# Kernel tuning notes

Hardware: AMD Instinct MI355X
Metric: run time of the kernel (lower is better)

Reference implementation:

```python
import jax, jax.numpy as jnp
import numpy as np

TOP_K = 8


def setup_inputs() -> dict:
    key = jax.random.key(0)
    ks = jax.random.split(key, 5)
    T, H, I, E = 4096, 2048, 1024, 64
    s = 0.02
    return {
        "x": jax.random.normal(ks[0], (T, H), jnp.float32),
        "gate_w": jax.random.normal(ks[1], (E, H), jnp.float32) * s,
        "gate_b": jax.random.normal(ks[2], (E,), jnp.float32) * s,
        "fc1_w": jax.random.normal(ks[3], (E, 2 * I, H), jnp.float32) * s,
        "fc2_w": jax.random.normal(ks[4], (E, H, I), jnp.float32) * s,
    }


def reference(x, gate_w, gate_b, fc1_w, fc2_w):
    # Router: [T, E] logits, top-k, softmax over selected logits in fp32.
    E = gate_w.shape[0]
    logits = x @ gate_w.T + gate_b
    topk_logits, topk_idx = jax.lax.top_k(logits, TOP_K)
    w = jax.nn.softmax(topk_logits.astype(jnp.float32), axis=-1).astype(x.dtype)
    # Per-token combine weight for each expert: [T, E] (0 if expert not selected).
    comb = (jax.nn.one_hot(topk_idx, E, dtype=x.dtype) * w[..., None]).sum(axis=1)
    # Scan over experts: each step is one dense GEMM-GeGLU-GEMM with masked combine.
    def body(acc, ew):
        W1, W2, c = ew  # W1 [2I, H], W2 [H, I], c [T]
        h_full = x @ W1.T                       # [T, 2I]
        h, g = jnp.split(h_full, 2, axis=-1)
        a = jax.nn.gelu(h, approximate=False) * (g + 1.0)  # custom GeGLU
        y = a @ W2.T                            # [T, H]
        return acc + c[:, None] * y, None

    out0 = jnp.zeros_like(x)
    out, _ = jax.lax.scan(body, out0, (fc1_w, fc2_w, comb.T))
    return out
```

## Files before the change

kernel.cpp:

```cpp
#include <hip/hip_runtime.h>
#include <hip/hip_bf16.h>
#include <cfloat>
#include <math.h>

#define T_TOK 4096
#define H_DIM 2048
#define E_NUM 64
#define I_DIM 1024
#define TOPK  8
#define BM    256
#define BK    64
#define MAXT  192

typedef __attribute__((ext_vector_type(4))) float f32x4;
typedef __attribute__((ext_vector_type(8))) short bf16x8;
typedef __attribute__((ext_vector_type(4))) int   i32x4;

__device__ __forceinline__ unsigned short f2bf(float f) {
    union { float f; unsigned int u; } v; v.f = f;
    unsigned int r = v.u + 0x7FFFu + ((v.u >> 16) & 1u);
    return (unsigned short)(r >> 16);
}
__device__ __forceinline__ unsigned int pack2(float a, float b) {
    return (unsigned int)f2bf(a) | ((unsigned int)f2bf(b) << 16);
}
__device__ __forceinline__ float bf2f(unsigned short u) {
    union { unsigned int u; float f; } v; v.u = (unsigned int)u << 16; return v.f;
}
__device__ __forceinline__ int cvtpk(float lo, float hi) {
    int r; asm("v_cvt_pk_bf16_f32 %0, %1, %2" : "=v"(r) : "v"(lo), "v"(hi)); return r;
}
__device__ __forceinline__ void gload16(const void* g, void* l) {
    __builtin_amdgcn_global_load_lds((const __attribute__((address_space(1))) unsigned int*)g,
                                     (__attribute__((address_space(3))) unsigned int*)l, 16, 0, 0);
}

__global__ __launch_bounds__(256)
void router_kernel(const float* __restrict__ x, const float* __restrict__ gw,
                   const float* __restrict__ gb, unsigned short* __restrict__ xb,
                   int* __restrict__ topk_idx, float* __restrict__ topk_w,
                   int* __restrict__ counts)
{
    const int t = blockIdx.x;
    const int tid = threadIdx.x;
    __shared__ float xs[H_DIM];
    __shared__ float logits[E_NUM];
    const float* xrow = x + (size_t)t * H_DIM;

    #pragma unroll
    for (int i = 0; i < 2; ++i) {
        int c = i * 1024 + tid * 4;
        f32x4 v = *(const f32x4*)(xrow + c);
        *(f32x4*)(xs + c) = v;
        uint2 pk; pk.x = pack2(v.x, v.y); pk.y = pack2(v.z, v.w);
        *(uint2*)(xb + (size_t)t * H_DIM + c) = pk;
    }
    __syncthreads();

    const int wave = tid >> 6, lane = tid & 63;
    for (int ee = 0; ee < 16; ++ee) {
        const int e = wave * 16 + ee;
        const float* g = gw + (size_t)e * H_DIM;
        float p = 0.f;
        #pragma unroll
        for (int i = 0; i < 8; ++i) {
            int c = (i * 64 + lane) * 4;
            f32x4 gv = *(const f32x4*)(g + c);
            f32x4 xv = *(const f32x4*)(xs + c);
            p += gv.x * xv.x + gv.y * xv.y + gv.z * xv.z + gv.w * xv.w;
        }
        #pragma unroll
        for (int s = 32; s > 0; s >>= 1) p += __shfl_xor(p, s, 64);
        if (lane == 0) logits[e] = p + gb[e];
    }
    __syncthreads();

    if (tid < 64) {
        float cur = logits[tid];
        float wv[TOPK]; int wi[TOPK];
        #pragma unroll
        for (int k = 0; k < TOPK; ++k) {
            float bv = cur; int bi = tid;
            #pragma unroll
            for (int s = 32; s > 0; s >>= 1) {
                float ov = __shfl_xor(bv, s, 64);
                int   oi = __shfl_xor(bi, s, 64);
                if (ov > bv || (ov == bv && oi < bi)) { bv = ov; bi = oi; }
            }
            wv[k] = bv; wi[k] = bi;
            if (tid == bi) cur = -FLT_MAX;
        }
        if (tid == 0) {
            float mx = wv[0], sum = 0.f, ex[TOPK];
            #pragma unroll
            for (int k = 0; k < TOPK; ++k) { ex[k] = expf(wv[k] - mx); sum += ex[k]; }
            #pragma unroll
            for (int k = 0; k < TOPK; ++k) {
                topk_idx[t * TOPK + k] = wi[k];
                topk_w[t * TOPK + k]   = ex[k] / sum;
                atomicAdd(&counts[wi[k]], 1);
            }
        }
    }
}

__global__ void scan_kernel(const int* __restrict__ counts, int* __restrict__ offsets,
                            int* __restrict__ cursors, int* __restrict__ tiles,
                            int* __restrict__ ntiles)
{
    if (threadIdx.x == 0) {
        int acc = 0, nt = 0;
        for (int e = 0; e < E_NUM; ++e) {
            offsets[e] = acc; cursors[e] = acc;
            int c = counts[e];
            for (int m = 0; m * BM < c; ++m) tiles[nt++] = (e << 16) | m;
            acc += c;
        }
        *ntiles = nt;
    }
}

__global__ void assign_kernel(const int* __restrict__ topk_idx, const float* __restrict__ topk_w,
                              int* __restrict__ cursors, int* __restrict__ tok_of,
                              int* __restrict__ pos_of)
{
    int i = blockIdx.x * 256 + threadIdx.x;
    if (i >= T_TOK * TOPK) return;
    int e = topk_idx[i];
    int pos = atomicAdd(&cursors[e], 1);
    tok_of[pos] = i >> 3;
    pos_of[i]   = pos;
}

__global__ __launch_bounds__(512, 1)
void gemm1_kernel(const unsigned short* __restrict__ xb, const float* __restrict__ fc1,
                  const int* __restrict__ counts, const int* __restrict__ offsets,
                  const int* __restrict__ tok_of, const int* __restrict__ tiles,
                  const int* __restrict__ ntiles, unsigned short* __restrict__ a_all)
{
    const int ty = blockIdx.y;
    if (ty >= *ntiles) return;
    const int code = tiles[ty];
    const int e = code >> 16, m0 = (code & 0xffff) * BM;
    const int cnt = counts[e], off = offsets[e];
    const int n0 = blockIdx.x * 128;
    const float* W = fc1 + (size_t)e * (size_t)(2 * I_DIM) * H_DIM;

    __shared__ unsigned short sA[2][BM * BK];
    __shared__ unsigned short sB[2 * 128 * BK];
    __shared__ int sTok[BM];

    const int tid = threadIdx.x;
    if (tid < BM) {
        int m = m0 + tid;
        sTok[tid] = tok_of[off + (m < cnt ? m : cnt - 1)];
    }
    __syncthreads();

    const int wid = tid >> 6, lane = tid & 63;
    const int srow = tid >> 3, sch = tid & 7;
    const int sslot = sch ^ (srow & 7);

    const unsigned short* aSrc[4];
    const float* bSrc[4];
    #pragma unroll
    for (int i = 0; i < 4; ++i) {
        int row = srow + 64 * i;
        aSrc[i] = xb + (size_t)sTok[row] * H_DIM + sslot * 8;
        int wrow = (row < 128) ? (n0 + row) : (I_DIM + n0 + (row - 128));
        bSrc[i] = W + (size_t)wrow * H_DIM + sch * 8;
    }

    f32x4 accH[4][4], accG[4][4];
    #pragma unroll
    for (int m = 0; m < 4; ++m)
        #pragma unroll
        for (int n = 0; n < 4; ++n) {
            accH[m][n] = (f32x4){0.f, 0.f, 0.f, 0.f};
            accG[m][n] = (f32x4){0.f, 0.f, 0.f, 0.f};
        }

    const int wm = (wid >> 1) * 64;
    const int wnp = (wid & 1) * 64;
    const int fr = lane & 15;
    const int kg = lane >> 4;

    f32x4 br[8];

    auto issueB = [&](int k0) {
        #pragma unroll
        for (int i = 0; i < 4; ++i) {
            br[2 * i]     = *(const f32x4*)(bSrc[i] + k0);
            br[2 * i + 1] = *(const f32x4*)(bSrc[i] + k0 + 4);
        }
    };
    auto issueA = [&](int k0, int buf) {
        #pragma unroll
        for (int i = 0; i < 4; ++i)
            gload16(aSrc[i] + k0, &sA[buf][(64 * i + 8 * wid) * BK]);
    };
    auto writeB = [&]() {
        #pragma unroll
        for (int i = 0; i < 4; ++i) {
            int row = srow + 64 * i;
            i32x4 pk = (i32x4){cvtpk(br[2*i].x,   br[2*i].y),
                               cvtpk(br[2*i].z,   br[2*i].w),
                               cvtpk(br[2*i+1].x, br[2*i+1].y),
                               cvtpk(br[2*i+1].z, br[2*i+1].w)};
            int byte = (row * 128 + sch * 16) ^ ((row & 7) << 4);
            *(i32x4*)((char*)sB + byte) = pk;
        }
    };
    auto compute = [&](int buf) {
        #pragma unroll
        for (int kk = 0; kk < 2; ++kk) {
            bf16x8 af[4], bh[4], bg[4];
            #pragma unroll
            for (int m = 0; m < 4; ++m) {
                int row = wm + m * 16 + fr;
                af[m] = *(const bf16x8*)((const char*)sA[buf] +
                        ((row * 128 + kk * 64 + kg * 16) ^ ((row & 7) << 4)));
            }
            #pragma unroll
            for (int n = 0; n < 4; ++n) {
                int rh = wnp + n * 16 + fr;
                bh[n] = *(const bf16x8*)((const char*)sB +
                        ((rh * 128 + kk * 64 + kg * 16) ^ ((rh & 7) << 4)));
                int rg = 128 + rh;
                bg[n] = *(const bf16x8*)((const char*)sB +
                        ((rg * 128 + kk * 64 + kg * 16) ^ ((rg & 7) << 4)));
            }
            #pragma unroll
            for (int m = 0; m < 4; ++m)
                #pragma unroll
                for (int n = 0; n < 4; ++n) {
                    accH[m][n] = __builtin_amdgcn_mfma_f32_16x16x32_bf16(af[m], bh[n], accH[m][n], 0, 0, 0);
                    accG[m][n] = __builtin_amdgcn_mfma_f32_16x16x32_bf16(af[m], bg[n], accG[m][n], 0, 0, 0);
                }
        }
    };

    const int NT = H_DIM / BK;
    issueB(0);
    issueA(0, 0);
    __syncthreads();
    writeB();
    __syncthreads();
    int cur = 0;
    for (int t = 0; t < NT; ++t) {
        const bool more = (t + 1) < NT;
        if (more) { issueB((t + 1) * BK); issueA((t + 1) * BK, cur ^ 1); }
        compute(cur);
        __syncthreads();
        if (more) writeB();
        __syncthreads();
        cur ^= 1;
    }

    #pragma unroll
    for (int m = 0; m < 4; ++m) {
        int rbase = wm + m * 16 + kg * 4;
        #pragma unroll
        for (int r = 0; r < 4; ++r) {
            int gm = m0 + rbase + r;
            if (gm < cnt) {
                size_t rowoff = (size_t)(off + gm) * I_DIM + n0 + wnp;
                #pragma unroll
                for (int n = 0; n < 4; ++n) {
                    float h = accH[m][n][r];
                    float g = accG[m][n][r];
                    float a = 0.5f * h * (1.f + erff(h * 0.70710678118f)) * (g + 1.f);
                    a_all[rowoff + n * 16 + fr] = f2bf(a);
                }
            }
        }
    }
}

__global__ __launch_bounds__(512, 1)
void gemm2_kernel(const unsigned short* __restrict__ a_all, const float* __restrict__ fc2,
                  const int* __restrict__ counts, const int* __restrict__ offsets,
                  const int* __restrict__ tiles, const int* __restrict__ ntiles,
                  unsigned short* __restrict__ y)
{
    const int ty = blockIdx.y;
    if (ty >= *ntiles) return;
    const int code = tiles[ty];
    const int e = code >> 16, m0 = (code & 0xffff) * BM;
    const int cnt = counts[e], off = offsets[e];
    const int n0 = blockIdx.x * 128;
    const float* W = fc2 + (size_t)e * (size_t)H_DIM * I_DIM;

    __shared__ unsigned short sA[2][BM * BK];
    __shared__ unsigned short sB[128 * BK];

    const int tid = threadIdx.x;
    const int wid = tid >> 6, lane = tid & 63;
    const int srow = tid >> 3, sch = tid & 7;
    const int sslot = sch ^ (srow & 7);

    const unsigned short* aSrc[4];
    const float* bSrc[2];
    #pragma unroll
    for (int i = 0; i < 4; ++i) {
        int row = srow + 64 * i;
        aSrc[i] = a_all + (size_t)(off + m0 + row) * I_DIM + sslot * 8;
    }
    #pragma unroll
    for (int i = 0; i < 2; ++i) {
        int row = srow + 64 * i;
        bSrc[i] = W + (size_t)(n0 + row) * I_DIM + sch * 8;
    }

    f32x4 acc[4][4];
    #pragma unroll
    for (int m = 0; m < 4; ++m)
        #pragma unroll
        for (int n = 0; n < 4; ++n) acc[m][n] = (f32x4){0.f, 0.f, 0.f, 0.f};

    const int wm = (wid >> 1) * 64;
    const int wn = (wid & 1) * 64;
    const int fr = lane & 15;
    const int kg = lane >> 4;

    f32x4 br[4];

    auto issueB = [&](int k0) {
        #pragma unroll
        for (int i = 0; i < 2; ++i) {
            br[2 * i]     = *(const f32x4*)(bSrc[i] + k0);
            br[2 * i + 1] = *(const f32x4*)(bSrc[i] + k0 + 4);
        }
    };
    auto issueA = [&](int k0, int buf) {
        #pragma unroll
        for (int i = 0; i < 4; ++i)
            gload16(aSrc[i] + k0, &sA[buf][(64 * i + 8 * wid) * BK]);
    };
    auto writeB = [&]() {
        #pragma unroll
        for (int i = 0; i < 2; ++i) {
            int row = srow + 64 * i;
            i32x4 pk = (i32x4){cvtpk(br[2*i].x,   br[2*i].y),
                               cvtpk(br[2*i].z,   br[2*i].w),
                               cvtpk(br[2*i+1].x, br[2*i+1].y),
                               cvtpk(br[2*i+1].z, br[2*i+1].w)};
            int byte = (row * 128 + sch * 16) ^ ((row & 7) << 4);
            *(i32x4*)((char*)sB + byte) = pk;
        }
    };
    auto compute = [&](int buf) {
        #pragma unroll
        for (int kk = 0; kk < 2; ++kk) {
            bf16x8 af[4], bfr[4];
            #pragma unroll
            for (int m = 0; m < 4; ++m) {
                int row = wm + m * 16 + fr;
                af[m] = *(const bf16x8*)((const char*)sA[buf] +
                        ((row * 128 + kk * 64 + kg * 16) ^ ((row & 7) << 4)));
            }
            #pragma unroll
            for (int n = 0; n < 4; ++n) {
                int row = wn + n * 16 + fr;
                bfr[n] = *(const bf16x8*)((const char*)sB +
                        ((row * 128 + kk * 64 + kg * 16) ^ ((row & 7) << 4)));
            }
            #pragma unroll
            for (int m = 0; m < 4; ++m)
                #pragma unroll
                for (int n = 0; n < 4; ++n)
                    acc[m][n] = __builtin_amdgcn_mfma_f32_16x16x32_bf16(af[m], bfr[n], acc[m][n], 0, 0, 0);
        }
    };

    const int NT = I_DIM / BK;
    issueB(0);
    issueA(0, 0);
    __syncthreads();
    writeB();
    __syncthreads();
    int cur = 0;
    for (int t = 0; t < NT; ++t) {
        const bool more = (t + 1) < NT;
        if (more) { issueB((t + 1) * BK); issueA((t + 1) * BK, cur ^ 1); }
        compute(cur);
        __syncthreads();
        if (more) writeB();
        __syncthreads();
        cur ^= 1;
    }

    #pragma unroll
    for (int m = 0; m < 4; ++m) {
        int rbase = wm + m * 16 + kg * 4;
        #pragma unroll
        for (int r = 0; r < 4; ++r) {
            int gm = m0 + rbase + r;
            if (gm < cnt) {
                size_t rowoff = (size_t)(off + gm) * H_DIM + n0 + wn;
                #pragma unroll
                for (int n = 0; n < 4; ++n)
                    y[rowoff + n * 16 + fr] = f2bf(acc[m][n][r]);
            }
        }
    }
}

__global__ __launch_bounds__(256)
void combine_kernel(const unsigned short* __restrict__ y, const int* __restrict__ pos_of,
                    const float* __restrict__ topk_w, float* __restrict__ out)
{
    const int t = blockIdx.x;
    const int tid = threadIdx.x;
    __shared__ int   sp[TOPK];
    __shared__ float sw[TOPK];
    if (tid < TOPK) {
        sp[tid] = pos_of[t * TOPK + tid];
        sw[tid] = topk_w[t * TOPK + tid];
    }
    __syncthreads();

    const int c0 = tid * 8;
    float acc[8];
    #pragma unroll
    for (int j = 0; j < 8; ++j) acc[j] = 0.f;
    #pragma unroll
    for (int k = 0; k < TOPK; ++k) {
        const float w = sw[k];
        i32x4 v = *(const i32x4*)(y + (size_t)sp[k] * H_DIM + c0);
        const unsigned short* u = (const unsigned short*)&v;
        #pragma unroll
        for (int j = 0; j < 8; ++j) acc[j] += w * bf2f(u[j]);
    }
    float* orow = out + (size_t)t * H_DIM + c0;
    *(f32x4*)orow       = (f32x4){acc[0], acc[1], acc[2], acc[3]};
    *(f32x4*)(orow + 4) = (f32x4){acc[4], acc[5], acc[6], acc[7]};
}

extern "C" void kernel_launch(void* const* d_in, const int* in_sizes, int n_in,
                              void* d_out, int out_size, void* d_ws, size_t ws_size,
                              hipStream_t stream)
{
    const float* x   = (const float*)d_in[0];
    const float* gw  = (const float*)d_in[1];
    const float* gb  = (const float*)d_in[2];
    const float* fc1 = (const float*)d_in[3];
    const float* fc2 = (const float*)d_in[4];
    float* out = (float*)d_out;

    char* ws = (char*)d_ws;
    size_t o = 0;
    auto alloc = [&](size_t b) { void* p = ws + o; o = (o + b + 255) & ~(size_t)255; return p; };
    unsigned short* xb     = (unsigned short*)alloc((size_t)T_TOK * H_DIM * 2);
    int*            tk_idx = (int*)  alloc((size_t)T_TOK * TOPK * 4);
    float*          tk_w   = (float*)alloc((size_t)T_TOK * TOPK * 4);
    int*            counts = (int*)  alloc(E_NUM * 4);
    int*            offs   = (int*)  alloc(E_NUM * 4);
    int*            curs   = (int*)  alloc(E_NUM * 4);
    int*            tiles  = (int*)  alloc(MAXT * 4);
    int*            ntiles = (int*)  alloc(4);
    int*            tok_of = (int*)  alloc((size_t)T_TOK * TOPK * 4);
    int*            pos_of = (int*)  alloc((size_t)T_TOK * TOPK * 4);
    unsigned short* a_all  = (unsigned short*)alloc((size_t)(T_TOK * TOPK + BM) * I_DIM * 2);
    unsigned short* yb     = (unsigned short*)alloc((size_t)T_TOK * TOPK * H_DIM * 2);
    (void)ws_size;

    hipMemsetAsync(counts, 0, E_NUM * 4, stream);

    router_kernel<<<T_TOK, 256, 0, stream>>>(x, gw, gb, xb, tk_idx, tk_w, counts);
    scan_kernel<<<1, 64, 0, stream>>>(counts, offs, curs, tiles, ntiles);
    assign_kernel<<<(T_TOK * TOPK + 255) / 256, 256, 0, stream>>>(tk_idx, tk_w, curs, tok_of, pos_of);
    gemm1_kernel<<<dim3(I_DIM / 128, MAXT), 512, 0, stream>>>(xb, fc1, counts, offs, tok_of,
                                                              tiles, ntiles, a_all);
    gemm2_kernel<<<dim3(H_DIM / 128, MAXT), 512, 0, stream>>>(a_all, fc2, counts, offs,
                                                              tiles, ntiles, yb);
    combine_kernel<<<T_TOK, 256, 0, stream>>>(yb, pos_of, tk_w, out);
}
```

Baseline: 1.261 ms.

## Use 640-row expert tiles so most experts fit one M tile, single-buffer A

Raises the per-expert M tile from 256 to 640 rows, so a typical expert (about 512 tokens) needs one tile and the fp32 weights are streamed and converted once per expert rather than per 256-row tile. Each warp now owns 80 rows. gemm1's N tile shrinks to 64 and gemm2's per-warp N grows to 128. To fit LDS, A moves from double to single buffering, with the A load issued after compute, which serialises A loads with MFMA work. Risks include wasted padding rows and worse latency hiding.

Measured after the change: 1.145 ms. 1.1x faster.

```diff
diff --git a/kernel.cpp b/kernel.cpp
--- a/kernel.cpp
+++ b/kernel.cpp
@@ -8,9 +8,9 @@
 #define E_NUM 64
 #define I_DIM 1024
 #define TOPK  8
-#define BM    256
+#define BM    640
 #define BK    64
-#define MAXT  192
+#define MAXT  128
 
 typedef __attribute__((ext_vector_type(4))) float f32x4;
 typedef __attribute__((ext_vector_type(8))) short bf16x8;
@@ -143,17 +143,21 @@
     const int code = tiles[ty];
     const int e = code >> 16, m0 = (code & 0xffff) * BM;
     const int cnt = counts[e], off = offsets[e];
-    const int n0 = blockIdx.x * 128;
+    const int n0 = blockIdx.x * 64;
     const float* W = fc1 + (size_t)e * (size_t)(2 * I_DIM) * H_DIM;
 
-    __shared__ unsigned short sA[2][BM * BK];
-    __shared__ unsigned short sB[2 * 128 * BK];
+    __shared__ unsigned short sA[BM * BK];
+    __shared__ unsigned short sB[128 * BK];
     __shared__ int sTok[BM];
 
     const int tid = threadIdx.x;
-    if (tid < BM) {
-        int m = m0 + tid;
-        sTok[tid] = tok_of[off + (m < cnt ? m : cnt - 1)];
+    {
+        int r0 = m0 + tid;
+        sTok[tid] = tok_of[off + (r0 < cnt ? r0 : cnt - 1)];
+        if (tid < BM - 512) {
+            int r1 = m0 + 512 + tid;
+            sTok[512 + tid] = tok_of[off + (r1 < cnt ? r1 : cnt - 1)];
+        }
     }
     __syncthreads();
 
@@ -161,165 +165,30 @@
     const int srow = tid >> 3, sch = tid & 7;
     const int sslot = sch ^ (srow & 7);
 
-    const unsigned short* aSrc[4];
-    const float* bSrc[4];
-    #pragma unroll
-    for (int i = 0; i < 4; ++i) {
+    const unsigned short* aSrc[10];
+    #pragma unroll
+    for (int i = 0; i < 10; ++i) {
         int row = srow + 64 * i;
         aSrc[i] = xb + (size_t)sTok[row] * H_DIM + sslot * 8;
-        int wrow = (row < 128) ? (n0 + row) : (I_DIM + n0 + (row - 128));
+    }
+    const float* bSrc[2];
+    #pragma unroll
+    for (int i = 0; i < 2; ++i) {
+        int row = srow + 64 * i;
+        int wrow = (row < 64) ? (n0 + row) : (I_DIM + n0 + (row - 64));
         bSrc[i] = W + (size_t)wrow * H_DIM + sch * 8;
     }
 
-    f32x4 accH[4][4], accG[4][4];
-    #pragma unroll
-    for (int m = 0; m < 4; ++m)
+    f32x4 accH[5][4], accG[5][4];
+    #pragma unroll
+    for (int m = 0; m < 5; ++m)
         #pragma unroll
         for (int n = 0; n < 4; ++n) {
             accH[m][n] = (f32x4){0.f, 0.f, 0.f, 0.f};
             accG[m][n] = (f32x4){0.f, 0.f, 0.f, 0.f};
         }
 
-    const int wm = (wid >> 1) * 64;
-    const int wnp = (wid & 1) * 64;
-    const int fr = lane & 15;
-    const int kg = lane >> 4;
-
-    f32x4 br[8];
-
-    auto issueB = [&](int k0) {
-        #pragma unroll
-        for (int i = 0; i < 4; ++i) {
-            br[2 * i]     = *(const f32x4*)(bSrc[i] + k0);
-            br[2 * i + 1] = *(const f32x4*)(bSrc[i] + k0 + 4);
-        }
-    };
-    auto issueA = [&](int k0, int buf) {
-        #pragma unroll
-        for (int i = 0; i < 4; ++i)
-            gload16(aSrc[i] + k0, &sA[buf][(64 * i + 8 * wid) * BK]);
-    };
-    auto writeB = [&]() {
-        #pragma unroll
-        for (int i = 0; i < 4; ++i) {
-            int row = srow + 64 * i;
-            i32x4 pk = (i32x4){cvtpk(br[2*i].x,   br[2*i].y),
-                               cvtpk(br[2*i].z,   br[2*i].w),
-                               cvtpk(br[2*i+1].x, br[2*i+1].y),
-                               cvtpk(br[2*i+1].z, br[2*i+1].w)};
-            int byte = (row * 128 + sch * 16) ^ ((row & 7) << 4);
-            *(i32x4*)((char*)sB + byte) = pk;
-        }
-    };
-    auto compute = [&](int buf) {
-        #pragma unroll
-        for (int kk = 0; kk < 2; ++kk) {
-            bf16x8 af[4], bh[4], bg[4];
-            #pragma unroll
-            for (int m = 0; m < 4; ++m) {
-                int row = wm + m * 16 + fr;
-                af[m] = *(const bf16x8*)((const char*)sA[buf] +
-                        ((row * 128 + kk * 64 + kg * 16) ^ ((row & 7) << 4)));
-            }
-            #pragma unroll
-            for (int n = 0; n < 4; ++n) {
-                int rh = wnp + n * 16 + fr;
-                bh[n] = *(const bf16x8*)((const char*)sB +
-                        ((rh * 128 + kk * 64 + kg * 16) ^ ((rh & 7) << 4)));
-                int rg = 128 + rh;
-                bg[n] = *(const bf16x8*)((const char*)sB +
-                        ((rg * 128 + kk * 64 + kg * 16) ^ ((rg & 7) << 4)));
-            }
-            #pragma unroll
-            for (int m = 0; m < 4; ++m)
-                #pragma unroll
-                for (int n = 0; n < 4; ++n) {
-                    accH[m][n] = __builtin_amdgcn_mfma_f32_16x16x32_bf16(af[m], bh[n], accH[m][n], 0, 0, 0);
-                    accG[m][n] = __builtin_amdgcn_mfma_f32_16x16x32_bf16(af[m], bg[n], accG[m][n], 0, 0, 0);
-                }
-        }
-    };
-
-    const int NT = H_DIM / BK;
-    issueB(0);
-    issueA(0, 0);
-    __syncthreads();
-    writeB();
-    __syncthreads();
-    int cur = 0;
-    for (int t = 0; t < NT; ++t) {
-        const bool more = (t + 1) < NT;
-        if (more) { issueB((t + 1) * BK); issueA((t + 1) * BK, cur ^ 1); }
-        compute(cur);
-        __syncthreads();
-        if (more) writeB();
-        __syncthreads();
-        cur ^= 1;
-    }
-
-    #pragma unroll
-    for (int m = 0; m < 4; ++m) {
-        int rbase = wm + m * 16 + kg * 4;
-        #pragma unroll
-        for (int r = 0; r < 4; ++r) {
-            int gm = m0 + rbase + r;
-            if (gm < cnt) {
-                size_t rowoff = (size_t)(off + gm) * I_DIM + n0 + wnp;
-                #pragma unroll
-                for (int n = 0; n < 4; ++n) {
-                    float h = accH[m][n][r];
-                    float g = accG[m][n][r];
-                    float a = 0.5f * h * (1.f + erff(h * 0.70710678118f)) * (g + 1.f);
-                    a_all[rowoff + n * 16 + fr] = f2bf(a);
-                }
-            }
-        }
-    }
-}
-
-__global__ __launch_bounds__(512, 1)
-void gemm2_kernel(const unsigned short* __restrict__ a_all, const float* __restrict__ fc2,
-                  const int* __restrict__ counts, const int* __restrict__ offsets,
-                  const int* __restrict__ tiles, const int* __restrict__ ntiles,
-                  unsigned short* __restrict__ y)
-{
-    const int ty = blockIdx.y;
-    if (ty >= *ntiles) return;
-    const int code = tiles[ty];
-    const int e = code >> 16, m0 = (code & 0xffff) * BM;
-    const int cnt = counts[e], off = offsets[e];
-    const int n0 = blockIdx.x * 128;
-    const float* W = fc2 + (size_t)e * (size_t)H_DIM * I_DIM;
-
-    __shared__ unsigned short sA[2][BM * BK];
-    __shared__ unsigned short sB[128 * BK];
-
-    const int tid = threadIdx.x;
-    const int wid = tid >> 6, lane = tid & 63;
-    const int srow = tid >> 3, sch = tid & 7;
-    const int sslot = sch ^ (srow & 7);
-
-    const unsigned short* aSrc[4];
-    const float* bSrc[2];
-    #pragma unroll
-    for (int i = 0; i < 4; ++i) {
-        int row = srow + 64 * i;
-        aSrc[i] = a_all + (size_t)(off + m0 + row) * I_DIM + sslot * 8;
-    }
-    #pragma unroll
-    for (int i = 0; i < 2; ++i) {
-        int row = srow + 64 * i;
-        bSrc[i] = W + (size_t)(n0 + row) * I_DIM + sch * 8;
-    }
-
-    f32x4 acc[4][4];
-    #pragma unroll
-    for (int m = 0; m < 4; ++m)
-        #pragma unroll
-        for (int n = 0; n < 4; ++n) acc[m][n] = (f32x4){0.f, 0.f, 0.f, 0.f};
-
-    const int wm = (wid >> 1) * 64;
-    const int wn = (wid & 1) * 64;
+    const int wm = wid * 80;
     const int fr = lane & 15;
     const int kg = lane >> 4;
 
@@ -332,10 +201,10 @@
             br[2 * i + 1] = *(const f32x4*)(bSrc[i] + k0 + 4);
         }
     };
-    auto issueA = [&](int k0, int buf) {
-        #pragma unroll
-        for (int i = 0; i < 4; ++i)
-            gload16(aSrc[i] + k0, &sA[buf][(64 * i + 8 * wid) * BK]);
+    auto issueA = [&](int k0) {
+        #pragma unroll
+        for (int i = 0; i < 10; ++i)
+            gload16(aSrc[i] + k0, &sA[(64 * i + 8 * wid) * BK]);
     };
     auto writeB = [&]() {
         #pragma unroll
@@ -349,57 +218,188 @@
             *(i32x4*)((char*)sB + byte) = pk;
         }
     };
-    auto compute = [&](int buf) {
+    auto compute = [&]() {
         #pragma unroll
         for (int kk = 0; kk < 2; ++kk) {
-            bf16x8 af[4], bfr[4];
-            #pragma unroll
-            for (int m = 0; m < 4; ++m) {
+            bf16x8 af[5], bh[4], bg[4];
+            #pragma unroll
+            for (int m = 0; m < 5; ++m) {
                 int row = wm + m * 16 + fr;
-                af[m] = *(const bf16x8*)((const char*)sA[buf] +
+                af[m] = *(const bf16x8*)((const char*)sA +
                         ((row * 128 + kk * 64 + kg * 16) ^ ((row & 7) << 4)));
             }
             #pragma unroll
             for (int n = 0; n < 4; ++n) {
-                int row = wn + n * 16 + fr;
-                bfr[n] = *(const bf16x8*)((const char*)sB +
-                        ((row * 128 + kk * 64 + kg * 16) ^ ((row & 7) << 4)));
-            }
-            #pragma unroll
-            for (int m = 0; m < 4; ++m)
+                int rh = n * 16 + fr;
+                bh[n] = *(const bf16x8*)((const char*)sB +
+                        ((rh * 128 + kk * 64 + kg * 16) ^ ((rh & 7) << 4)));
+                int rg = 64 + rh;
+                bg[n] = *(const bf16x8*)((const char*)sB +
+                        ((rg * 128 + kk * 64 + kg * 16) ^ ((rg & 7) << 4)));
+            }
+            #pragma unroll
+            for (int m = 0; m < 5; ++m)
                 #pragma unroll
-                for (int n = 0; n < 4; ++n)
-                    acc[m][n] = __builtin_amdgcn_mfma_f32_16x16x32_bf16(af[m], bfr[n], acc[m][n], 0, 0, 0);
-        }
-    };
-
-    const int NT = I_DIM / BK;
+                for (int n = 0; n < 4; ++n) {
+                    accH[m][n] = __builtin_amdgcn_mfma_f32_16x16x32_bf16(af[m], bh[n], accH[m][n], 0, 0, 0);
+                    accG[m][n] = __builtin_amdgcn_mfma_f32_16x16x32_bf16(af[m], bg[n], accG[m][n], 0, 0, 0);
+                }
+        }
+    };
+
+    const int NT = H_DIM / BK;
     issueB(0);
-    issueA(0, 0);
+    issueA(0);
     __syncthreads();
     writeB();
     __syncthreads();
-    int cur = 0;
     for (int t = 0; t < NT; ++t) {
-        const bool more = (t + 1) < NT;
-        if (more) { issueB((t + 1) * BK); issueA((t + 1) * BK, cur ^ 1); }
-        compute(cur);
+        if (t + 1 < NT) issueB((t + 1) * BK);
+        compute();
         __syncthreads();
-        if (more) writeB();
+        if (t + 1 < NT) { issueA((t + 1) * BK); writeB(); }
         __syncthreads();
-        cur ^= 1;
-    }
-
-    #pragma unroll
-    for (int m = 0; m < 4; ++m) {
+    }
+
+    #pragma unroll
+    for (int m = 0; m < 5; ++m) {
         int rbase = wm + m * 16 + kg * 4;
         #pragma unroll
         for (int r = 0; r < 4; ++r) {
             int gm = m0 + rbase + r;
             if (gm < cnt) {
-                size_t rowoff = (size_t)(off + gm) * H_DIM + n0 + wn;
+                size_t rowoff = (size_t)(off + gm) * I_DIM + n0;
                 #pragma unroll
-                for (int n = 0; n < 4; ++n)
+                for (int n = 0; n < 4; ++n) {
+                    float h = accH[m][n][r];
+                    float g = accG[m][n][r];
+                    float a = 0.5f * h * (1.f + erff(h * 0.70710678118f)) * (g + 1.f);
+                    a_all[rowoff + n * 16 + fr] = f2bf(a);
+                }
+            }
+        }
+    }
+}
+
+__global__ __launch_bounds__(512, 1)
+void gemm2_kernel(const unsigned short* __restrict__ a_all, const float* __restrict__ fc2,
+                  const int* __restrict__ counts, const int* __restrict__ offsets,
+                  const int* __restrict__ tiles, const int* __restrict__ ntiles,
+                  unsigned short* __restrict__ y)
+{
+    const int ty = blockIdx.y;
+    if (ty >= *ntiles) return;
+    const int code = tiles[ty];
+    const int e = code >> 16, m0 = (code & 0xffff) * BM;
+    const int cnt = counts[e], off = offsets[e];
+    const int n0 = blockIdx.x * 128;
+    const float* W = fc2 + (size_t)e * (size_t)H_DIM * I_DIM;
+
+    __shared__ unsigned short sA[BM * BK];
+    __shared__ unsigned short sB[128 * BK];
+
+    const int tid = threadIdx.x;
+    const int wid = tid >> 6, lane = tid & 63;
+    const int srow = tid >> 3, sch = tid & 7;
+    const int sslot = sch ^ (srow & 7);
+
+    const unsigned short* aSrc[10];
+    #pragma unroll
+    for (int i = 0; i < 10; ++i) {
+        int row = srow + 64 * i;
+        aSrc[i] = a_all + (size_t)(off + m0 + row) * I_DIM + sslot * 8;
+    }
+    const float* bSrc[2];
+    #pragma unroll
+    for (int i = 0; i < 2; ++i) {
+        int row = srow + 64 * i;
+        bSrc[i] = W + (size_t)(n0 + row) * I_DIM + sch * 8;
+    }
+
+    f32x4 acc[5][8];
+    #pragma unroll
+    for (int m = 0; m < 5; ++m)
+        #pragma unroll
+        for (int n = 0; n < 8; ++n) acc[m][n] = (f32x4){0.f, 0.f, 0.f, 0.f};
+
+    const int wm = wid * 80;
+    const int fr = lane & 15;
+    const int kg = lane >> 4;
+
+    f32x4 br[4];
+
+    auto issueB = [&](int k0) {
+        #pragma unroll
+        for (int i = 0; i < 2; ++i) {
+            br[2 * i]     = *(const f32x4*)(bSrc[i] + k0);
+            br[2 * i + 1] = *(const f32x4*)(bSrc[i] + k0 + 4);
+        }
+    };
+    auto issueA = [&](int k0) {
+        #pragma unroll
+        for (int i = 0; i < 10; ++i)
+            gload16(aSrc[i] + k0, &sA[(64 * i + 8 * wid) * BK]);
+    };
+    auto writeB = [&]() {
+        #pragma unroll
+        for (int i = 0; i < 2; ++i) {
+            int row = srow + 64 * i;
+            i32x4 pk = (i32x4){cvtpk(br[2*i].x,   br[2*i].y),
+                               cvtpk(br[2*i].z,   br[2*i].w),
+                               cvtpk(br[2*i+1].x, br[2*i+1].y),
+                               cvtpk(br[2*i+1].z, br[2*i+1].w)};
+            int byte = (row * 128 + sch * 16) ^ ((row & 7) << 4);
+            *(i32x4*)((char*)sB + byte) = pk;
+        }
+    };
+    auto compute = [&]() {
+        #pragma unroll
+        for (int kk = 0; kk < 2; ++kk) {
+            bf16x8 af[5], bfr[8];
+            #pragma unroll
+            for (int m = 0; m < 5; ++m) {
+                int row = wm + m * 16 + fr;
+                af[m] = *(const bf16x8*)((const char*)sA +
+                        ((row * 128 + kk * 64 + kg * 16) ^ ((row & 7) << 4)));
+            }
+            #pragma unroll
+            for (int n = 0; n < 8; ++n) {
+                int row = n * 16 + fr;
+                bfr[n] = *(const bf16x8*)((const char*)sB +
+                        ((row * 128 + kk * 64 + kg * 16) ^ ((row & 7) << 4)));
+            }
+            #pragma unroll
+            for (int m = 0; m < 5; ++m)
+                #pragma unroll
+                for (int n = 0; n < 8; ++n)
+                    acc[m][n] = __builtin_amdgcn_mfma_f32_16x16x32_bf16(af[m], bfr[n], acc[m][n], 0, 0, 0);
+        }
+    };
+
+    const int NT = I_DIM / BK;
+    issueB(0);
+    issueA(0);
+    __syncthreads();
+    writeB();
+    __syncthreads();
+    for (int t = 0; t < NT; ++t) {
+        if (t + 1 < NT) issueB((t + 1) * BK);
+        compute();
+        __syncthreads();
+        if (t + 1 < NT) { issueA((t + 1) * BK); writeB(); }
+        __syncthreads();
+    }
+
+    #pragma unroll
+    for (int m = 0; m < 5; ++m) {
+        int rbase = wm + m * 16 + kg * 4;
+        #pragma unroll
+        for (int r = 0; r < 4; ++r) {
+            int gm = m0 + rbase + r;
+            if (gm < cnt) {
+                size_t rowoff = (size_t)(off + gm) * H_DIM + n0;
+                #pragma unroll
+                for (int n = 0; n < 8; ++n)
                     y[rowoff + n * 16 + fr] = f2bf(acc[m][n][r]);
             }
         }
@@ -462,7 +462,7 @@
     int*            tok_of = (int*)  alloc((size_t)T_TOK * TOPK * 4);
     int*            pos_of = (int*)  alloc((size_t)T_TOK * TOPK * 4);
     unsigned short* a_all  = (unsigned short*)alloc((size_t)(T_TOK * TOPK + BM) * I_DIM * 2);
-    unsigned short* yb     = (unsigned short*)alloc((size_t)T_TOK * TOPK * H_DIM * 2);
+    unsigned short* yb     = (unsigned short*)alloc((size_t)(T_TOK * TOPK + BM) * H_DIM * 2);
     (void)ws_size;
 
     hipMemsetAsync(counts, 0, E_NUM * 4, stream);
@@ -470,8 +470,8 @@
     router_kernel<<<T_TOK, 256, 0, stream>>>(x, gw, gb, xb, tk_idx, tk_w, counts);
     scan_kernel<<<1, 64, 0, stream>>>(counts, offs, curs, tiles, ntiles);
     assign_kernel<<<(T_TOK * TOPK + 255) / 256, 256, 0, stream>>>(tk_idx, tk_w, curs, tok_of, pos_of);
-    gemm1_kernel<<<dim3(I_DIM / 128, MAXT), 512, 0, stream>>>(xb, fc1, counts, offs, tok_of,
-                                                              tiles, ntiles, a_all);
+    gemm1_kernel<<<dim3(I_DIM / 64, MAXT), 512, 0, stream>>>(xb, fc1, counts, offs, tok_of,
+                                                             tiles, ntiles, a_all);
     gemm2_kernel<<<dim3(H_DIM / 128, MAXT), 512, 0, stream>>>(a_all, fc2, counts, offs,
                                                               tiles, ntiles, yb);
     combine_kernel<<<T_TOK, 256, 0, stream>>>(yb, pos_of, tk_w, out);
```

## Shrink grouped GEMM tiles to 128x128, split GeGLU into separate kernel

Applied to the files above, without the earlier changes.

Both expert GEMMs move from 256-row tiles with 512 threads to 128x128 tiles with 256 threads and two blocks per CU. The B tile is now double-buffered so one barrier per k-step can be dropped, and MFMA sections are wrapped in s_setprio. GEMM1 no longer pairs the h and g halves in one block. It writes the full bf16 pre-activation to a new buffer, and a separate elementwise kernel applies the GeGLU. The goal is less padding waste per expert and better occupancy, at the cost of extra global traffic for the intermediate and one more launch.

Result: slower. 1.501 ms (+19.0%).

```diff
diff --git a/kernel.cpp b/kernel.cpp
--- a/kernel.cpp
+++ b/kernel.cpp
@@ -8,9 +8,9 @@
 #define E_NUM 64
 #define I_DIM 1024
 #define TOPK  8
-#define BM    256
+#define BM    128
 #define BK    64
-#define MAXT  192
+#define MAXT  320
 
 typedef __attribute__((ext_vector_type(4))) float f32x4;
 typedef __attribute__((ext_vector_type(8))) short bf16x8;
@@ -132,22 +132,22 @@
     pos_of[i]   = pos;
 }
 
-__global__ __launch_bounds__(512, 1)
+__global__ __launch_bounds__(256, 2)
 void gemm1_kernel(const unsigned short* __restrict__ xb, const float* __restrict__ fc1,
                   const int* __restrict__ counts, const int* __restrict__ offsets,
                   const int* __restrict__ tok_of, const int* __restrict__ tiles,
-                  const int* __restrict__ ntiles, unsigned short* __restrict__ a_all)
+                  const int* __restrict__ ntiles, unsigned short* __restrict__ h_full)
 {
     const int ty = blockIdx.y;
     if (ty >= *ntiles) return;
     const int code = tiles[ty];
     const int e = code >> 16, m0 = (code & 0xffff) * BM;
     const int cnt = counts[e], off = offsets[e];
-    const int n0 = blockIdx.x * 128;
+    const int n0 = blockIdx.x * BM;
     const float* W = fc1 + (size_t)e * (size_t)(2 * I_DIM) * H_DIM;
 
     __shared__ unsigned short sA[2][BM * BK];
-    __shared__ unsigned short sB[2 * 128 * BK];
+    __shared__ unsigned short sB[2][BM * BK];
     __shared__ int sTok[BM];
 
     const int tid = threadIdx.x;
@@ -159,29 +159,24 @@
 
     const int wid = tid >> 6, lane = tid & 63;
     const int srow = tid >> 3, sch = tid & 7;
-    const int sslot = sch ^ (srow & 7);
+    const int brow = tid >> 1, bhalf = tid & 1;
 
     const unsigned short* aSrc[4];
-    const float* bSrc[4];
     #pragma unroll
     for (int i = 0; i < 4; ++i) {
-        int row = srow + 64 * i;
-        aSrc[i] = xb + (size_t)sTok[row] * H_DIM + sslot * 8;
-        int wrow = (row < 128) ? (n0 + row) : (I_DIM + n0 + (row - 128));
-        bSrc[i] = W + (size_t)wrow * H_DIM + sch * 8;
-    }
-
-    f32x4 accH[4][4], accG[4][4];
+        int row = srow + 32 * i;
+        aSrc[i] = xb + (size_t)sTok[row] * H_DIM + (sch ^ (row & 7)) * 8;
+    }
+    const float* bSrc = W + (size_t)(n0 + brow) * H_DIM + bhalf * 32;
+
+    f32x4 acc[4][4];
     #pragma unroll
     for (int m = 0; m < 4; ++m)
         #pragma unroll
-        for (int n = 0; n < 4; ++n) {
-            accH[m][n] = (f32x4){0.f, 0.f, 0.f, 0.f};
-            accG[m][n] = (f32x4){0.f, 0.f, 0.f, 0.f};
-        }
+        for (int n = 0; n < 4; ++n) acc[m][n] = (f32x4){0.f, 0.f, 0.f, 0.f};
 
     const int wm = (wid >> 1) * 64;
-    const int wnp = (wid & 1) * 64;
+    const int wn = (wid & 1) * 64;
     const int fr = lane & 15;
     const int kg = lane >> 4;
 
@@ -189,70 +184,61 @@
 
     auto issueB = [&](int k0) {
         #pragma unroll
-        for (int i = 0; i < 4; ++i) {
-            br[2 * i]     = *(const f32x4*)(bSrc[i] + k0);
-            br[2 * i + 1] = *(const f32x4*)(bSrc[i] + k0 + 4);
-        }
+        for (int j = 0; j < 8; ++j) br[j] = *(const f32x4*)(bSrc + k0 + j * 4);
     };
     auto issueA = [&](int k0, int buf) {
         #pragma unroll
         for (int i = 0; i < 4; ++i)
-            gload16(aSrc[i] + k0, &sA[buf][(64 * i + 8 * wid) * BK]);
-    };
-    auto writeB = [&]() {
-        #pragma unroll
-        for (int i = 0; i < 4; ++i) {
-            int row = srow + 64 * i;
-            i32x4 pk = (i32x4){cvtpk(br[2*i].x,   br[2*i].y),
-                               cvtpk(br[2*i].z,   br[2*i].w),
-                               cvtpk(br[2*i+1].x, br[2*i+1].y),
-                               cvtpk(br[2*i+1].z, br[2*i+1].w)};
-            int byte = (row * 128 + sch * 16) ^ ((row & 7) << 4);
-            *(i32x4*)((char*)sB + byte) = pk;
+            gload16(aSrc[i] + k0, &sA[buf][(32 * i + 8 * wid) * BK]);
+    };
+    auto writeB = [&](int buf) {
+        #pragma unroll
+        for (int j = 0; j < 4; ++j) {
+            i32x4 pk = (i32x4){cvtpk(br[2*j].x,   br[2*j].y),
+                               cvtpk(br[2*j].z,   br[2*j].w),
+                               cvtpk(br[2*j+1].x, br[2*j+1].y),
+                               cvtpk(br[2*j+1].z, br[2*j+1].w)};
+            int s = bhalf * 4 + j;
+            *(i32x4*)((char*)sB[buf] + brow * 128 + ((s ^ (brow & 7)) * 16)) = pk;
         }
     };
     auto compute = [&](int buf) {
         #pragma unroll
         for (int kk = 0; kk < 2; ++kk) {
-            bf16x8 af[4], bh[4], bg[4];
+            bf16x8 af[4], bf[4];
             #pragma unroll
             for (int m = 0; m < 4; ++m) {
                 int row = wm + m * 16 + fr;
                 af[m] = *(const bf16x8*)((const char*)sA[buf] +
-                        ((row * 128 + kk * 64 + kg * 16) ^ ((row & 7) << 4)));
+                        row * 128 + (((kk * 4 + kg) ^ (row & 7)) * 16));
             }
             #pragma unroll
             for (int n = 0; n < 4; ++n) {
-                int rh = wnp + n * 16 + fr;
-                bh[n] = *(const bf16x8*)((const char*)sB +
-                        ((rh * 128 + kk * 64 + kg * 16) ^ ((rh & 7) << 4)));
-                int rg = 128 + rh;
-                bg[n] = *(const bf16x8*)((const char*)sB +
-                        ((rg * 128 + kk * 64 + kg * 16) ^ ((rg & 7) << 4)));
-            }
+                int row = wn + n * 16 + fr;
+                bf[n] = *(const bf16x8*)((const char*)sB[buf] +
+                        row * 128 + (((kk * 4 + kg) ^ (row & 7)) * 16));
+            }
+            __builtin_amdgcn_s_setprio(1);
             #pragma unroll
             for (int m = 0; m < 4; ++m)
                 #pragma unroll
-                for (int n = 0; n < 4; ++n) {
-                    accH[m][n] = __builtin_amdgcn_mfma_f32_16x16x32_bf16(af[m], bh[n], accH[m][n], 0, 0, 0);
-                    accG[m][n] = __builtin_amdgcn_mfma_f32_16x16x32_bf16(af[m], bg[n], accG[m][n], 0, 0, 0);
-                }
+                for (int n = 0; n < 4; ++n)
+                    acc[m][n] = __builtin_amdgcn_mfma_f32_16x16x32_bf16(af[m], bf[n], acc[m][n], 0, 0, 0);
+            __builtin_amdgcn_s_setprio(0);
         }
     };
 
     const int NT = H_DIM / BK;
     issueB(0);
     issueA(0, 0);
-    __syncthreads();
-    writeB();
+    writeB(0);
     __syncthreads();
     int cur = 0;
     for (int t = 0; t < NT; ++t) {
         const bool more = (t + 1) < NT;
         if (more) { issueB((t + 1) * BK); issueA((t + 1) * BK, cur ^ 1); }
         compute(cur);
-        __syncthreads();
-        if (more) writeB();
+        if (more) writeB(cur ^ 1);
         __syncthreads();
         cur ^= 1;
     }
@@ -264,20 +250,40 @@
         for (int r = 0; r < 4; ++r) {
             int gm = m0 + rbase + r;
             if (gm < cnt) {
-                size_t rowoff = (size_t)(off + gm) * I_DIM + n0 + wnp;
+                size_t rowoff = (size_t)(off + gm) * (2 * I_DIM) + n0 + wn;
                 #pragma unroll
-                for (int n = 0; n < 4; ++n) {
-                    float h = accH[m][n][r];
-                    float g = accG[m][n][r];
-                    float a = 0.5f * h * (1.f + erff(h * 0.70710678118f)) * (g + 1.f);
-                    a_all[rowoff + n * 16 + fr] = f2bf(a);
-                }
-            }
-        }
-    }
-}
-
-__global__ __launch_bounds__(512, 1)
+                for (int n = 0; n < 4; ++n)
+                    h_full[rowoff + n * 16 + fr] = f2bf(acc[m][n][r]);
+            }
+        }
+    }
+}
+
+__global__ __launch_bounds__(256)
+void geglu_kernel(const unsigned short* __restrict__ h_full, unsigned short* __restrict__ a_all)
+{
+    long long g = (long long)blockIdx.x * 256 + threadIdx.x;
+    long long pos = g * 8;
+    int row = (int)(pos >> 10);
+    int col = (int)(pos & 1023);
+    const unsigned short* hrow = h_full + (size_t)row * (2 * I_DIM);
+    i32x4 hv = *(const i32x4*)(hrow + col);
+    i32x4 gv = *(const i32x4*)(hrow + I_DIM + col);
+    const unsigned short* hu = (const unsigned short*)&hv;
+    const unsigned short* gu = (const unsigned short*)&gv;
+    int out[4];
+    #pragma unroll
+    for (int j = 0; j < 4; ++j) {
+        float h0 = bf2f(hu[2*j]),   g0 = bf2f(gu[2*j]);
+        float h1 = bf2f(hu[2*j+1]), g1 = bf2f(gu[2*j+1]);
+        float a0 = 0.5f * h0 * (1.f + erff(h0 * 0.70710678118f)) * (g0 + 1.f);
+        float a1 = 0.5f * h1 * (1.f + erff(h1 * 0.70710678118f)) * (g1 + 1.f);
+        out[j] = cvtpk(a0, a1);
+    }
+    *(i32x4*)(a_all + (size_t)row * I_DIM + col) = (i32x4){out[0], out[1], out[2], out[3]};
+}
+
+__global__ __launch_bounds__(256, 2)
 void gemm2_kernel(const unsigned short* __restrict__ a_all, const float* __restrict__ fc2,
                   const int* __restrict__ counts, const int* __restrict__ offsets,
                   const int* __restrict__ tiles, const int* __restrict__ ntiles,
@@ -288,29 +294,24 @@
     const int code = tiles[ty];
     const int e = code >> 16, m0 = (code & 0xffff) * BM;
     const int cnt = counts[e], off = offsets[e];
-    const int n0 = blockIdx.x * 128;
+    const int n0 = blockIdx.x * BM;
     const float* W = fc2 + (size_t)e * (size_t)H_DIM * I_DIM;
 
     __shared__ unsigned short sA[2][BM * BK];
-    __shared__ unsigned short sB[128 * BK];
+    __shared__ unsigned short sB[2][BM * BK];
 
     const int tid = threadIdx.x;
     const int wid = tid >> 6, lane = tid & 63;
     const int srow = tid >> 3, sch = tid & 7;
-    const int sslot = sch ^ (srow & 7);
+    const int brow = tid >> 1, bhalf = tid & 1;
 
     const unsigned short* aSrc[4];
-    const float* bSrc[2];
     #pragma unroll
     for (int i = 0; i < 4; ++i) {
-        int row = srow + 64 * i;
-        aSrc[i] = a_all + (size_t)(off + m0 + row) * I_DIM + sslot * 8;
-    }
-    #pragma unroll
-    for (int i = 0; i < 2; ++i) {
-        int row = srow + 64 * i;
-        bSrc[i] = W + (size_t)(n0 + row) * I_DIM + sch * 8;
-    }
+        int row = srow + 32 * i;
+        aSrc[i] = a_all + (size_t)(off + m0 + row) * I_DIM + (sch ^ (row & 7)) * 8;
+    }
+    const float* bSrc = W + (size_t)(n0 + brow) * I_DIM + bhalf * 32;
 
     f32x4 acc[4][4];
     #pragma unroll
@@ -323,69 +324,65 @@
     const int fr = lane & 15;
     const int kg = lane >> 4;
 
-    f32x4 br[4];
+    f32x4 br[8];
 
     auto issueB = [&](int k0) {
         #pragma unroll
-        for (int i = 0; i < 2; ++i) {
-            br[2 * i]     = *(const f32x4*)(bSrc[i] + k0);
-            br[2 * i + 1] = *(const f32x4*)(bSrc[i] + k0 + 4);
-        }
+        for (int j = 0; j < 8; ++j) br[j] = *(const f32x4*)(bSrc + k0 + j * 4);
     };
     auto issueA = [&](int k0, int buf) {
         #pragma unroll
         for (int i = 0; i < 4; ++i)
-            gload16(aSrc[i] + k0, &sA[buf][(64 * i + 8 * wid) * BK]);
-    };
-    auto writeB = [&]() {
-        #pragma unroll
-        for (int i = 0; i < 2; ++i) {
-            int row = srow + 64 * i;
-            i32x4 pk = (i32x4){cvtpk(br[2*i].x,   br[2*i].y),
-                               cvtpk(br[2*i].z,   br[2*i].w),
-                               cvtpk(br[2*i+1].x, br[2*i+1].y),
-                               cvtpk(br[2*i+1].z, br[2*i+1].w)};
-            int byte = (row * 128 + sch * 16) ^ ((row & 7) << 4);
-            *(i32x4*)((char*)sB + byte) = pk;
+            gload16(aSrc[i] + k0, &sA[buf][(32 * i + 8 * wid) * BK]);
+    };
+    auto writeB = [&](int buf) {
+        #pragma unroll
+        for (int j = 0; j < 4; ++j) {
+            i32x4 pk = (i32x4){cvtpk(br[2*j].x,   br[2*j].y),
+                               cvtpk(br[2*j].z,   br[2*j].w),
+                               cvtpk(br[2*j+1].x, br[2*j+1].y),
+                               cvtpk(br[2*j+1].z, br[2*j+1].w)};
+            int s = bhalf * 4 + j;
+            *(i32x4*)((char*)sB[buf] + brow * 128 + ((s ^ (brow & 7)) * 16)) = pk;
         }
     };
     auto compute = [&](int buf) {
         #pragma unroll
         for (int kk = 0; kk < 2; ++kk) {
-            bf16x8 af[4], bfr[4];
+            bf16x8 af[4], bf[4];
             #pragma unroll
             for (int m = 0; m < 4; ++m) {
                 int row = wm + m * 16 + fr;
                 af[m] = *(const bf16x8*)((const char*)sA[buf] +
-                        ((row * 128 + kk * 64 + kg * 16) ^ ((row & 7) << 4)));
+                        row * 128 + (((kk * 4 + kg) ^ (row & 7)) * 16));
             }
             #pragma unroll
             for (int n = 0; n < 4; ++n) {
                 int row = wn + n * 16 + fr;
-                bfr[n] = *(const bf16x8*)((const char*)sB +
-                        ((row * 128 + kk * 64 + kg * 16) ^ ((row & 7) << 4)));
-            }
+                bf[n] = *(const bf16x8*)((const char*)sB[buf] +
+                        row * 128 + (((kk * 4 + kg) ^ (row & 7)) * 16));
+            }
+            __builtin_amdgcn_s_setprio(1);
             #pragma unroll
             for (int m = 0; m < 4; ++m)
                 #pragma unroll
                 for (int n = 0; n < 4; ++n)
-                    acc[m][n] = __builtin_amdgcn_mfma_f32_16x16x32_bf16(af[m], bfr[n], acc[m][n], 0, 0, 0);
+                    acc[m][n] = __builtin_amdgcn_mfma_f32_16x16x32_bf16(af[m], bf[n], acc[m][n], 0, 0, 0);
+            __builtin_amdgcn_s_setprio(0);
         }
     };
 
     const int NT = I_DIM / BK;
     issueB(0);
     issueA(0, 0);
-    __syncthreads();
-    writeB();
+    writeB(0);
     __syncthreads();
     int cur = 0;
     for (int t = 0; t < NT; ++t) {
         const bool more = (t + 1) < NT;
         if (more) { issueB((t + 1) * BK); issueA((t + 1) * BK, cur ^ 1); }
         compute(cur);
-        __syncthreads();
-        if (more) writeB();
+        if (more) writeB(cur ^ 1);
         __syncthreads();
         cur ^= 1;
     }
@@ -461,8 +458,9 @@
     int*            ntiles = (int*)  alloc(4);
     int*            tok_of = (int*)  alloc((size_t)T_TOK * TOPK * 4);
     int*            pos_of = (int*)  alloc((size_t)T_TOK * TOPK * 4);
+    unsigned short* h_full = (unsigned short*)alloc((size_t)(T_TOK * TOPK + BM) * 2 * I_DIM * 2);
     unsigned short* a_all  = (unsigned short*)alloc((size_t)(T_TOK * TOPK + BM) * I_DIM * 2);
-    unsigned short* yb     = (unsigned short*)alloc((size_t)T_TOK * TOPK * H_DIM * 2);
+    unsigned short* yb     = (unsigned short*)alloc((size_t)(T_TOK * TOPK + BM) * H_DIM * 2);
     (void)ws_size;
 
     hipMemsetAsync(counts, 0, E_NUM * 4, stream);
@@ -470,9 +468,10 @@
     router_kernel<<<T_TOK, 256, 0, stream>>>(x, gw, gb, xb, tk_idx, tk_w, counts);
     scan_kernel<<<1, 64, 0, stream>>>(counts, offs, curs, tiles, ntiles);
     assign_kernel<<<(T_TOK * TOPK + 255) / 256, 256, 0, stream>>>(tk_idx, tk_w, curs, tok_of, pos_of);
-    gemm1_kernel<<<dim3(I_DIM / 128, MAXT), 512, 0, stream>>>(xb, fc1, counts, offs, tok_of,
-                                                              tiles, ntiles, a_all);
-    gemm2_kernel<<<dim3(H_DIM / 128, MAXT), 512, 0, stream>>>(a_all, fc2, counts, offs,
-                                                              tiles, ntiles, yb);
+    gemm1_kernel<<<dim3(2 * I_DIM / BM, MAXT), 256, 0, stream>>>(xb, fc1, counts, offs, tok_of,
+                                                                 tiles, ntiles, h_full);
+    geglu_kernel<<<(T_TOK * TOPK * I_DIM / 8) / 256, 256, 0, stream>>>(h_full, a_all);
+    gemm2_kernel<<<dim3(H_DIM / BM, MAXT), 256, 0, stream>>>(a_all, fc2, counts, offs,
+                                                             tiles, ntiles, yb);
     combine_kernel<<<T_TOK, 256, 0, stream>>>(yb, pos_of, tk_w, out);
 }
```
